# Optimization experiments

Measured on AMD Instinct MI355X. Metric: run time of the kernel, lower is better.

The kernel has to match this reference:

```python
import jax, jax.numpy as jnp
import numpy as np

H = 4
NEG_SLOPE = 0.2
N_P, N_A = 100000, 100000
E = 500000
L = 200000
F_IN, F_HID, F_OUT = 128, 128, 64


def setup_inputs() -> dict:
    key = jax.random.key(0)
    ks = jax.random.split(key, 32)
    s = 0.1  # weight init scale
    inp = {
        'x_paper': jax.random.normal(ks[0], (N_P, F_IN), jnp.float32),
        'x_author': jax.random.normal(ks[1], (N_A, F_IN), jnp.float32),
        'ei_pa': jax.random.randint(ks[2], (2, E), 0, N_P, jnp.int32),
        'ei_ap': jax.random.randint(ks[3], (2, E), 0, N_A, jnp.int32),
        'edge_label_index': jax.random.randint(ks[4], (2, L), 0, N_P, jnp.int32),
        # layer 1 params
        'p1W': s * jax.random.normal(ks[5], (F_IN, F_HID), jnp.float32),
        'p1b': jnp.zeros((F_HID,), jnp.float32),
        'a1W': s * jax.random.normal(ks[6], (F_IN, F_HID), jnp.float32),
        'a1b': jnp.zeros((F_HID,), jnp.float32),
        's1pa': s * jax.random.normal(ks[7], (H, F_HID // H), jnp.float32),
        'd1pa': s * jax.random.normal(ks[8], (H, F_HID // H), jnp.float32),
        's1ap': s * jax.random.normal(ks[9], (H, F_HID // H), jnp.float32),
        'd1ap': s * jax.random.normal(ks[10], (H, F_HID // H), jnp.float32),
        'k1W': s * jax.random.normal(ks[11], (F_HID, F_HID), jnp.float32),
        'k1b': jnp.zeros((F_HID,), jnp.float32),
        'q1': s * jax.random.normal(ks[12], (F_HID,), jnp.float32),
        # layer 2 params
        'p2W': s * jax.random.normal(ks[13], (F_HID, F_OUT), jnp.float32),
        'p2b': jnp.zeros((F_OUT,), jnp.float32),
        'a2W': s * jax.random.normal(ks[14], (F_HID, F_OUT), jnp.float32),
        'a2b': jnp.zeros((F_OUT,), jnp.float32),
        's2pa': s * jax.random.normal(ks[15], (H, F_OUT // H), jnp.float32),
        'd2pa': s * jax.random.normal(ks[16], (H, F_OUT // H), jnp.float32),
        's2ap': s * jax.random.normal(ks[17], (H, F_OUT // H), jnp.float32),
        'd2ap': s * jax.random.normal(ks[18], (H, F_OUT // H), jnp.float32),
        'k2W': s * jax.random.normal(ks[19], (F_OUT, F_OUT), jnp.float32),
        'k2b': jnp.zeros((F_OUT,), jnp.float32),
        'q2': s * jax.random.normal(ks[20], (F_OUT,), jnp.float32),
    }
    return inp


def _edge_attn(h_src, h_dst, src, dst, a_src, a_dst, num_dst):
    # h_*: [N, H, D]; a_*: [H, D]. Per-edge node-level GAT-style attention.
    alpha = (jnp.einsum('nhd,hd->nh', h_src, a_src)[src]
             + jnp.einsum('nhd,hd->nh', h_dst, a_dst)[dst])  # [E, H]
    alpha = jnp.where(alpha >= 0, alpha, NEG_SLOPE * alpha)  # leaky_relu
    amax = jax.ops.segment_max(alpha, dst, num_segments=num_dst)
    amax = jnp.where(jnp.isfinite(amax), amax, 0.0)
    ex = jnp.exp(alpha - amax[dst])
    denom = jax.ops.segment_sum(ex, dst, num_segments=num_dst)
    w = ex / (denom[dst] + 1e-16)
    out = jax.ops.segment_sum(h_src[src] * w[:, :, None], dst, num_segments=num_dst)
    return jax.nn.relu(out).reshape(num_dst, -1)  # [N_dst, H*D]


def _group(xs, q, kW, kb):
    # Semantic-level attention over metapaths (PyG HANConv `group`).
    out = jnp.stack(xs)  # [M, N, F]
    score = (q * jnp.tanh(out @ kW + kb).mean(axis=1)).sum(-1)  # [M]
    attn = jax.nn.softmax(score)
    return (attn[:, None, None] * out).sum(0)


def _han_layer(x_p, x_a, ei_pa, ei_ap, pW, pb, aW, ab, s_pa, d_pa, s_ap, d_ap, kW, kb, q):
    D = pW.shape[1] // H
    h_p = (x_p @ pW + pb).reshape(-1, H, D)
    h_a = (x_a @ aW + ab).reshape(-1, H, D)
    out_a = _edge_attn(h_p, h_a, ei_pa[0], ei_pa[1], s_pa, d_pa, h_a.shape[0])
    out_p = _edge_attn(h_a, h_p, ei_ap[0], ei_ap[1], s_ap, d_ap, h_p.shape[0])
    z_p = _group([out_p], q, kW, kb)
    z_a = _group([out_a], q, kW, kb)
    return z_p, z_a


def reference(x_paper, x_author, ei_pa, ei_ap, edge_label_index,
              p1W, p1b, a1W, a1b, s1pa, d1pa, s1ap, d1ap, k1W, k1b, q1,
              p2W, p2b, a2W, a2b, s2pa, d2pa, s2ap, d2ap, k2W, k2b, q2):
    z_p, z_a = _han_layer(x_paper, x_author, ei_pa, ei_ap,
                          p1W, p1b, a1W, a1b, s1pa, d1pa, s1ap, d1ap, k1W, k1b, q1)
    z_p, z_a = _han_layer(z_p, z_a, ei_pa, ei_ap,
                          p2W, p2b, a2W, a2b, s2pa, d2pa, s2ap, d2ap, k2W, k2b, q2)
    src = z_p[edge_label_index[0]]
    dst = z_a[edge_label_index[1]]
    return (src * dst).sum(axis=-1)  # [L]
```

## Files before the change

### kernel.cpp

```cpp
#include <hip/hip_runtime.h>


#define HEADS 4

typedef _Float16 f16x8 __attribute__((ext_vector_type(8)));
typedef _Float16 f16x4 __attribute__((ext_vector_type(4)));
typedef float    f32x4 __attribute__((ext_vector_type(4)));

__device__ __forceinline__ float leaky02(float a) {
    return a >= 0.f ? a : 0.2f * a;
}

__device__ __forceinline__ void prep_one(const float* W, _Float16* Wf, int M, int o) {
    const int NT = M / 16;
    const int v = o & 7, lane = (o >> 3) & 63, jt = o >> 9;
    const int t = jt / NT, j = jt % NT;
    const int k = t * 32 + (lane >> 4) * 8 + v;
    const int n = j * 16 + (lane & 15);
    Wf[o] = (_Float16)W[k * M + n];
}

__global__ __launch_bounds__(256) void prep_w4(
    const float* __restrict__ W1, _Float16* __restrict__ Wf1,
    const float* __restrict__ W2, _Float16* __restrict__ Wf2,
    const float* __restrict__ W3, _Float16* __restrict__ Wf3,
    const float* __restrict__ W4, _Float16* __restrict__ Wf4) {
    int o = blockIdx.x * 256 + threadIdx.x;
    if (o < 16384)       prep_one(W1, Wf1, 128, o);
    else if (o < 32768)  prep_one(W2, Wf2, 128, o - 16384);
    else if (o < 40960)  prep_one(W3, Wf3, 64, o - 32768);
    else if (o < 49152)  prep_one(W4, Wf4, 64, o - 40960);
}

template<int M, bool AHALF>
__global__ __launch_bounds__(256) void gemm_mfma_dual(
    const void* __restrict__ XA, const _Float16* __restrict__ WfA,
    const float* __restrict__ bA, _Float16* __restrict__ outA,
    const void* __restrict__ XB, const _Float16* __restrict__ WfB,
    const float* __restrict__ bB, _Float16* __restrict__ outB,
    int N, int nbHalf) {
    constexpr int NT = M / 16;
    __shared__ _Float16 stage[4][16][M + 4];

    const bool second = blockIdx.x >= nbHalf;
    const void* __restrict__ X        = second ? XB : XA;
    const _Float16* __restrict__ Wf   = second ? WfB : WfA;
    const float* __restrict__ b       = second ? bB : bA;
    _Float16* __restrict__ out        = second ? outB : outA;
    const int brow = second ? blockIdx.x - nbHalf : blockIdx.x;

    const int wave = threadIdx.x >> 6;
    const int lane = threadIdx.x & 63;
    const int row0 = (brow * 4 + wave) * 16;
    const int m    = lane & 15;
    const int quad = lane >> 4;

    f32x4 acc[NT];
    #pragma unroll
    for (int j = 0; j < NT; ++j) acc[j] = (f32x4){0.f, 0.f, 0.f, 0.f};

    int arow = row0 + m;
    if (arow >= N) arow = N - 1;

    #pragma unroll
    for (int t = 0; t < 4; ++t) {
        const int k0 = t * 32 + quad * 8;
        f16x8 a;
        if (AHALF) {
            a = *(const f16x8*)((const _Float16*)X + (size_t)arow * 128 + k0);
        } else {
            const float* xp = (const float*)X + (size_t)arow * 128 + k0;
            float4 v0 = *(const float4*)xp;
            float4 v1 = *(const float4*)(xp + 4);
            a = (f16x8){(_Float16)v0.x, (_Float16)v0.y, (_Float16)v0.z, (_Float16)v0.w,
                        (_Float16)v1.x, (_Float16)v1.y, (_Float16)v1.z, (_Float16)v1.w};
        }
        #pragma unroll
        for (int j = 0; j < NT; ++j) {
            f16x8 bf = *(const f16x8*)(Wf + ((size_t)(t * NT + j) * 64 + lane) * 8);
            acc[j] = __builtin_amdgcn_mfma_f32_16x16x32_f16(a, bf, acc[j], 0, 0, 0);
        }
    }

    #pragma unroll
    for (int j = 0; j < NT; ++j) {
        const float bias = b[j * 16 + m];
        #pragma unroll
        for (int r = 0; r < 4; ++r)
            stage[wave][quad * 4 + r][j * 16 + m] = (_Float16)(acc[j][r] + bias);
    }
    __syncthreads();

    constexpr int LPR = M / 4;
    constexpr int RPI = 64 / LPR;
    const int lr = lane % LPR;
    const int rq = lane / LPR;
    #pragma unroll
    for (int i = 0; i < 16 / RPI; ++i) {
        const int rr = i * RPI + rq;
        const int grow = row0 + rr;
        if (grow < N) {
            f16x4 v = *(const f16x4*)(&stage[wave][rr][lr * 4]);
            *(f16x4*)(out + (size_t)grow * M + lr * 4) = v;
        }
    }
}

template<int F, int D>
__global__ __launch_bounds__(256) void node_alpha_dual(
    const _Float16* __restrict__ hP, const float* __restrict__ sP,
    const float* __restrict__ dP, float* __restrict__ asP, float* __restrict__ adP,
    const _Float16* __restrict__ hA, const float* __restrict__ sA,
    const float* __restrict__ dA, float* __restrict__ asA, float* __restrict__ adA,
    int N) {
    constexpr int LPN = F / 4;
    constexpr int LPH = D / 4;
    const int gid    = blockIdx.x * blockDim.x + threadIdx.x;
    const int node_g = gid / LPN;
    const int lane   = gid % LPN;
    if (node_g >= 2 * N) return;
    const bool aut = node_g >= N;
    const int node = aut ? node_g - N : node_g;
    const _Float16* hbuf = aut ? hA : hP;
    const float* sv_p = aut ? sA : sP;
    const float* dv_p = aut ? dA : dP;
    float* as_p = aut ? asA : asP;
    float* ad_p = aut ? adA : adP;

    const int f0 = lane * 4;
    f16x4 h4 = *(const f16x4*)(hbuf + (size_t)node * F + f0);
    float4 sv = *(const float4*)(sv_p + f0);
    float4 dv = *(const float4*)(dv_p + f0);
    const float h0 = (float)h4[0], h1 = (float)h4[1], h2 = (float)h4[2], h3 = (float)h4[3];
    float ps = h0 * sv.x + h1 * sv.y + h2 * sv.z + h3 * sv.w;
    float pd = h0 * dv.x + h1 * dv.y + h2 * dv.z + h3 * dv.w;
    #pragma unroll
    for (int off = LPH >> 1; off > 0; off >>= 1) {
        ps += __shfl_xor(ps, off);
        pd += __shfl_xor(pd, off);
    }
    if ((lane % LPH) == 0) {
        int h = lane / LPH;
        as_p[(size_t)node * HEADS + h] = ps;
        ad_p[(size_t)node * HEADS + h] = pd;
    }
}

__global__ __launch_bounds__(256) void hist_dual(
    const int* __restrict__ dst_pa, const int* __restrict__ dst_ap,
    int* __restrict__ counts, int N, int E) {
    const int eg = blockIdx.x * 256 + threadIdx.x;
    if (eg >= 2 * E) return;
    const int idx = (eg < E) ? dst_pa[eg] : (N + dst_ap[eg - E]);
    atomicAdd(counts + idx, 1);
}

__global__ __launch_bounds__(256) void scan_blk(
    const int* __restrict__ in, int* __restrict__ out,
    int* __restrict__ bsum, int N) {
    __shared__ int sh[256];
    const int base = blockIdx.x * 1024 + threadIdx.x * 4;
    int v[4]; int s = 0;
    #pragma unroll
    for (int j = 0; j < 4; ++j) { v[j] = (base + j < N) ? in[base + j] : 0; s += v[j]; }
    sh[threadIdx.x] = s;
    __syncthreads();
    for (int off = 1; off < 256; off <<= 1) {
        int t = (threadIdx.x >= off) ? sh[threadIdx.x - off] : 0;
        __syncthreads();
        sh[threadIdx.x] += t;
        __syncthreads();
    }
    int run = sh[threadIdx.x] - s;
    #pragma unroll
    for (int j = 0; j < 4; ++j) {
        if (base + j < N) out[base + j] = run;
        run += v[j];
    }
    if (threadIdx.x == 255) bsum[blockIdx.x] = sh[255];
}

__global__ __launch_bounds__(256) void scan_sums(int* __restrict__ bsum, int nb) {
    __shared__ int sh[256];
    int v = (threadIdx.x < nb) ? bsum[threadIdx.x] : 0;
    sh[threadIdx.x] = v;
    __syncthreads();
    for (int off = 1; off < 256; off <<= 1) {
        int t = (threadIdx.x >= off) ? sh[threadIdx.x - off] : 0;
        __syncthreads();
        sh[threadIdx.x] += t;
        __syncthreads();
    }
    if (threadIdx.x < nb) bsum[threadIdx.x] = sh[threadIdx.x] - v;
}

__global__ __launch_bounds__(256) void scan_add(
    int* __restrict__ out, const int* __restrict__ bsum, int N) {
    const int base = blockIdx.x * 1024 + threadIdx.x * 4;
    const int add = bsum[blockIdx.x];
    #pragma unroll
    for (int j = 0; j < 4; ++j)
        if (base + j < N) out[base + j] += add;
}

__global__ __launch_bounds__(256) void scatter_dual(
    const int* __restrict__ src_pa, const int* __restrict__ dst_pa,
    const int* __restrict__ src_ap, const int* __restrict__ dst_ap,
    const int* __restrict__ offsets, int* __restrict__ cursor,
    int* __restrict__ perm, int N, int E) {
    const int eg = blockIdx.x * 256 + threadIdx.x;
    if (eg >= 2 * E) return;
    int idx, val;
    if (eg < E) { idx = dst_pa[eg];         val = src_pa[eg]; }
    else        { idx = N + dst_ap[eg - E]; val = src_ap[eg - E]; }
    const int pos = offsets[idx] + atomicAdd(cursor + idx, 1);
    perm[pos] = val;
}

template<int F, int D>
__global__ __launch_bounds__(256) void csr_attn_agg_dual(
    const int* __restrict__ perm, const int* __restrict__ offsets,
    const int* __restrict__ counts,
    const float* __restrict__ asrcP, const float* __restrict__ adstP,
    const _Float16* __restrict__ hP, _Float16* __restrict__ outA,
    const float* __restrict__ asrcA, const float* __restrict__ adstA,
    const _Float16* __restrict__ hA, _Float16* __restrict__ outP,
    int N) {
    constexpr int LPN = F / 4;
    const int gid    = blockIdx.x * 256 + threadIdx.x;
    const int node_g = gid / LPN;
    const int lane   = gid % LPN;
    if (node_g >= 2 * N) return;
    const bool second = node_g >= N;
    const int node = second ? node_g - N : node_g;
    const float* __restrict__ asrc    = second ? asrcA : asrcP;
    const float* __restrict__ adst    = second ? adstA : adstP;
    const _Float16* __restrict__ hsrc = second ? hA : hP;
    _Float16* __restrict__ out        = second ? outP : outA;

    const int start = offsets[node_g];
    const int cnt   = counts[node_g];
    const int f0 = lane * 4;
    const int h  = f0 / D;
    const float ad = adst[(size_t)node * HEADS + h];

    float den = 0.f;
    float4 acc = make_float4(0.f, 0.f, 0.f, 0.f);
    for (int i = 0; i < cnt; ++i) {
        int s = perm[start + i];
        float a = leaky02(asrc[(size_t)s * HEADS + h] + ad);
        float ex = __expf(a);
        den += ex;
        f16x4 hv = *(const f16x4*)(hsrc + (size_t)s * F + f0);
        acc.x += ex * (float)hv[0]; acc.y += ex * (float)hv[1];
        acc.z += ex * (float)hv[2]; acc.w += ex * (float)hv[3];
    }
    const float inv = 1.f / (den + 1e-16f);
    f16x4 o;
    o[0] = (_Float16)fmaxf(acc.x * inv, 0.f);
    o[1] = (_Float16)fmaxf(acc.y * inv, 0.f);
    o[2] = (_Float16)fmaxf(acc.z * inv, 0.f);
    o[3] = (_Float16)fmaxf(acc.w * inv, 0.f);
    *(f16x4*)(out + (size_t)node * F + f0) = o;
}

__global__ __launch_bounds__(256) void edge_dot(
    const int* __restrict__ eli, const _Float16* __restrict__ zp,
    const _Float16* __restrict__ za, float* __restrict__ out, int L) {
    constexpr int LPE = 16;
    const int gid  = blockIdx.x * blockDim.x + threadIdx.x;
    const int e    = gid / LPE;
    const int lane = gid % LPE;
    if (e >= L) return;
    const int p = eli[e], a = eli[(size_t)L + e];
    f16x4 pv = *(const f16x4*)(zp + (size_t)p * 64 + lane * 4);
    f16x4 av = *(const f16x4*)(za + (size_t)a * 64 + lane * 4);
    float s = (float)pv[0] * (float)av[0] + (float)pv[1] * (float)av[1]
            + (float)pv[2] * (float)av[2] + (float)pv[3] * (float)av[3];
    #pragma unroll
    for (int off = 8; off > 0; off >>= 1) s += __shfl_xor(s, off);
    if (lane == 0) out[e] = s;
}

static inline int cdiv(long long a, long long b) { return (int)((a + b - 1) / b); }

extern "C" void kernel_launch(void* const* d_in, const int* in_sizes, int n_in,
                              void* d_out, int out_size, void* d_ws, size_t ws_size,
                              hipStream_t stream) {
    const float* x_p  = (const float*)d_in[0];
    const float* x_a  = (const float*)d_in[1];
    const int* ei_pa  = (const int*)d_in[2];
    const int* ei_ap  = (const int*)d_in[3];
    const int* eli    = (const int*)d_in[4];
    const float* p1W = (const float*)d_in[5];
    const float* p1b = (const float*)d_in[6];
    const float* a1W = (const float*)d_in[7];
    const float* a1b = (const float*)d_in[8];
    const float* s1pa = (const float*)d_in[9];
    const float* d1pa = (const float*)d_in[10];
    const float* s1ap = (const float*)d_in[11];
    const float* d1ap = (const float*)d_in[12];
    const float* p2W = (const float*)d_in[16];
    const float* p2b = (const float*)d_in[17];
    const float* a2W = (const float*)d_in[18];
    const float* a2b = (const float*)d_in[19];
    const float* s2pa = (const float*)d_in[20];
    const float* d2pa = (const float*)d_in[21];
    const float* s2ap = (const float*)d_in[22];
    const float* d2ap = (const float*)d_in[23];

    const int NP = in_sizes[0] / 128;
    const int E  = in_sizes[2] / 2;
    const int L  = in_sizes[4] / 2;
    const int N  = NP;

    char* ws = (char*)d_ws;
    size_t off = 0;
    auto alloc = [&](size_t bytes) -> char* {
        char* p = ws + off;
        off += (bytes + 255) & ~(size_t)255;
        return p;
    };
    _Float16* h_p1   = (_Float16*)alloc((size_t)N * 128 * 2);
    _Float16* h_a1   = (_Float16*)alloc((size_t)N * 128 * 2);
    _Float16* out_p1 = (_Float16*)alloc((size_t)N * 128 * 2);
    _Float16* out_a1 = (_Float16*)alloc((size_t)N * 128 * 2);
    _Float16* h_p2   = (_Float16*)alloc((size_t)N * 64 * 2);
    _Float16* h_a2   = (_Float16*)alloc((size_t)N * 64 * 2);
    _Float16* out_p2 = (_Float16*)alloc((size_t)N * 64 * 2);
    _Float16* out_a2 = (_Float16*)alloc((size_t)N * 64 * 2);
    float* asrc_pa = (float*)alloc((size_t)N * HEADS * 4);
    float* adst_pa = (float*)alloc((size_t)N * HEADS * 4);
    float* asrc_ap = (float*)alloc((size_t)N * HEADS * 4);
    float* adst_ap = (float*)alloc((size_t)N * HEADS * 4);
    _Float16* Wf1p = (_Float16*)alloc(16384 * 2);
    _Float16* Wf1a = (_Float16*)alloc(16384 * 2);
    _Float16* Wf2p = (_Float16*)alloc(8192 * 2);
    _Float16* Wf2a = (_Float16*)alloc(8192 * 2);
    int* cnt2    = (int*)alloc((size_t)2 * N * 4);
    int* cursor2 = (int*)alloc((size_t)2 * N * 4);
    int* off2    = (int*)alloc((size_t)2 * N * 4);
    int* perm2   = (int*)alloc((size_t)2 * E * 4);
    int* bsum    = (int*)alloc(256 * 4);

    const int* src_pa = ei_pa;
    const int* dst_pa = ei_pa + E;
    const int* src_ap = ei_ap;
    const int* dst_ap = ei_ap + E;

    const int N2 = 2 * N;
    const int nbScan = cdiv(N2, 1024);

    prep_w4<<<cdiv(49152, 256), 256, 0, stream>>>(p1W, Wf1p, a1W, Wf1a, p2W, Wf2p, a2W, Wf2a);
    hipMemsetAsync(cnt2, 0, (size_t)4 * N * 4, stream);
    hist_dual<<<cdiv((long long)2 * E, 256), 256, 0, stream>>>(dst_pa, dst_ap, cnt2, N, E);
    scan_blk<<<nbScan, 256, 0, stream>>>(cnt2, off2, bsum, N2);
    scan_sums<<<1, 256, 0, stream>>>(bsum, nbScan);
    scan_add<<<nbScan, 256, 0, stream>>>(off2, bsum, N2);
    scatter_dual<<<cdiv((long long)2 * E, 256), 256, 0, stream>>>(
        src_pa, dst_pa, src_ap, dst_ap, off2, cursor2, perm2, N, E);

    const int nbHalf = cdiv(N, 64);

    gemm_mfma_dual<128, false><<<2 * nbHalf, 256, 0, stream>>>(
        x_p, Wf1p, p1b, h_p1, x_a, Wf1a, a1b, h_a1, N, nbHalf);
    node_alpha_dual<128, 32><<<cdiv((long long)N2 * 32, 256), 256, 0, stream>>>(
        h_p1, s1pa, d1ap, asrc_pa, adst_ap,
        h_a1, s1ap, d1pa, asrc_ap, adst_pa, N);
    csr_attn_agg_dual<128, 32><<<cdiv((long long)N2 * 32, 256), 256, 0, stream>>>(
        perm2, off2, cnt2,
        asrc_pa, adst_pa, h_p1, out_a1,
        asrc_ap, adst_ap, h_a1, out_p1, N);

    gemm_mfma_dual<64, true><<<2 * nbHalf, 256, 0, stream>>>(
        out_p1, Wf2p, p2b, h_p2, out_a1, Wf2a, a2b, h_a2, N, nbHalf);
    node_alpha_dual<64, 16><<<cdiv((long long)N2 * 16, 256), 256, 0, stream>>>(
        h_p2, s2pa, d2ap, asrc_pa, adst_ap,
        h_a2, s2ap, d2pa, asrc_ap, adst_pa, N);
    csr_attn_agg_dual<64, 16><<<cdiv((long long)N2 * 16, 256), 256, 0, stream>>>(
        perm2, off2, cnt2,
        asrc_pa, adst_pa, h_p2, out_a2,
        asrc_ap, adst_ap, h_a2, out_p2, N);

    edge_dot<<<cdiv((long long)L * 16, 256), 256, 0, stream>>>(
        eli, out_p2, out_a2, (float*)d_out, L);
}
```

Before: 476.2 us.

## Fuse node attention logits into GEMM, degree-sort aggregation, unroll edge loop

The per-node attention logit computation moves into the GEMM epilogue, reading the staged fp16 tile from shared memory, and the separate node_alpha kernels are removed. That saves a launch and a full re-read of h per layer. A degree counting sort (histogram, scan, scatter) builds a node order so aggregation threads in the same wave handle nodes of similar in-degree, which reduces divergence. The aggregation edge loop is unrolled by four to put more gathers in flight. In exchange the change adds three small kernels. The GEMM epilogue drops the __syncthreads, which relies on each wave reading only its own stage slice. The bhist buffer is assumed contiguous after cursor2 so the memset clears it.

```diff
diff --git a/kernel.cpp b/kernel.cpp
--- a/kernel.cpp
+++ b/kernel.cpp
@@ -36,17 +36,26 @@
 __global__ __launch_bounds__(256) void gemm_mfma_dual(
     const void* __restrict__ XA, const _Float16* __restrict__ WfA,
     const float* __restrict__ bA, _Float16* __restrict__ outA,
+    const float* __restrict__ svA, const float* __restrict__ dvA,
+    float* __restrict__ asA, float* __restrict__ adA,
     const void* __restrict__ XB, const _Float16* __restrict__ WfB,
     const float* __restrict__ bB, _Float16* __restrict__ outB,
+    const float* __restrict__ svB, const float* __restrict__ dvB,
+    float* __restrict__ asB, float* __restrict__ adB,
     int N, int nbHalf) {
     constexpr int NT = M / 16;
+    constexpr int D  = M / HEADS;
     __shared__ _Float16 stage[4][16][M + 4];
 
     const bool second = blockIdx.x >= nbHalf;
-    const void* __restrict__ X        = second ? XB : XA;
-    const _Float16* __restrict__ Wf   = second ? WfB : WfA;
-    const float* __restrict__ b       = second ? bB : bA;
-    _Float16* __restrict__ out        = second ? outB : outA;
+    const void* __restrict__ X      = second ? XB : XA;
+    const _Float16* __restrict__ Wf = second ? WfB : WfA;
+    const float* __restrict__ b     = second ? bB : bA;
+    _Float16* __restrict__ out      = second ? outB : outA;
+    const float* __restrict__ sv    = second ? svB : svA;
+    const float* __restrict__ dv    = second ? dvB : dvA;
+    float* __restrict__ asb         = second ? asB : asA;
+    float* __restrict__ adb         = second ? adB : adA;
     const int brow = second ? blockIdx.x - nbHalf : blockIdx.x;
 
     const int wave = threadIdx.x >> 6;
@@ -89,7 +98,27 @@
         for (int r = 0; r < 4; ++r)
             stage[wave][quad * 4 + r][j * 16 + m] = (_Float16)(acc[j][r] + bias);
     }
-    __syncthreads();
+
+    {
+        const int r  = lane >> 2;
+        const int hh = lane & 3;
+        float ps = 0.f, pd = 0.f;
+        #pragma unroll
+        for (int j = 0; j < D / 4; ++j) {
+            f16x4 v4 = *(const f16x4*)(&stage[wave][r][hh * D + 4 * j]);
+            float4 s4 = *(const float4*)(sv + hh * D + 4 * j);
+            float4 d4 = *(const float4*)(dv + hh * D + 4 * j);
+            const float v0 = (float)v4[0], v1 = (float)v4[1],
+                        v2 = (float)v4[2], v3 = (float)v4[3];
+            ps += v0 * s4.x + v1 * s4.y + v2 * s4.z + v3 * s4.w;
+            pd += v0 * d4.x + v1 * d4.y + v2 * d4.z + v3 * d4.w;
+        }
+        const int grow = row0 + r;
+        if (grow < N) {
+            asb[(size_t)grow * HEADS + hh] = ps;
+            adb[(size_t)grow * HEADS + hh] = pd;
+        }
+    }
 
     constexpr int LPR = M / 4;
     constexpr int RPI = 64 / LPR;
@@ -103,46 +132,6 @@
             f16x4 v = *(const f16x4*)(&stage[wave][rr][lr * 4]);
             *(f16x4*)(out + (size_t)grow * M + lr * 4) = v;
         }
-    }
-}
-
-template<int F, int D>
-__global__ __launch_bounds__(256) void node_alpha_dual(
-    const _Float16* __restrict__ hP, const float* __restrict__ sP,
-    const float* __restrict__ dP, float* __restrict__ asP, float* __restrict__ adP,
-    const _Float16* __restrict__ hA, const float* __restrict__ sA,
-    const float* __restrict__ dA, float* __restrict__ asA, float* __restrict__ adA,
-    int N) {
-    constexpr int LPN = F / 4;
-    constexpr int LPH = D / 4;
-    const int gid    = blockIdx.x * blockDim.x + threadIdx.x;
-    const int node_g = gid / LPN;
-    const int lane   = gid % LPN;
-    if (node_g >= 2 * N) return;
-    const bool aut = node_g >= N;
-    const int node = aut ? node_g - N : node_g;
-    const _Float16* hbuf = aut ? hA : hP;
-    const float* sv_p = aut ? sA : sP;
-    const float* dv_p = aut ? dA : dP;
-    float* as_p = aut ? asA : asP;
-    float* ad_p = aut ? adA : adP;
-
-    const int f0 = lane * 4;
-    f16x4 h4 = *(const f16x4*)(hbuf + (size_t)node * F + f0);
-    float4 sv = *(const float4*)(sv_p + f0);
-    float4 dv = *(const float4*)(dv_p + f0);
-    const float h0 = (float)h4[0], h1 = (float)h4[1], h2 = (float)h4[2], h3 = (float)h4[3];
-    float ps = h0 * sv.x + h1 * sv.y + h2 * sv.z + h3 * sv.w;
-    float pd = h0 * dv.x + h1 * dv.y + h2 * dv.z + h3 * dv.w;
-    #pragma unroll
-    for (int off = LPH >> 1; off > 0; off >>= 1) {
-        ps += __shfl_xor(ps, off);
-        pd += __shfl_xor(pd, off);
-    }
-    if ((lane % LPH) == 0) {
-        int h = lane / LPH;
-        as_p[(size_t)node * HEADS + h] = ps;
-        ad_p[(size_t)node * HEADS + h] = pd;
     }
 }
 
@@ -217,8 +206,42 @@
     perm[pos] = val;
 }
 
+__global__ __launch_bounds__(256) void deg_hist(
+    const int* __restrict__ cnt, int* __restrict__ bhist, int n) {
+    __shared__ int lh[64];
+    if (threadIdx.x < 64) lh[threadIdx.x] = 0;
+    __syncthreads();
+    for (int i = blockIdx.x * 256 + threadIdx.x; i < n; i += gridDim.x * 256) {
+        int c = cnt[i]; if (c > 63) c = 63;
+        atomicAdd(&lh[c], 1);
+    }
+    __syncthreads();
+    if (threadIdx.x < 64) atomicAdd(&bhist[threadIdx.x], lh[threadIdx.x]);
+}
+
+__global__ __launch_bounds__(256) void deg_scatter(
+    const int* __restrict__ cnt, int* __restrict__ bcur,
+    int* __restrict__ order, int n) {
+    __shared__ int lh[64];
+    __shared__ int lbase[64];
+    if (threadIdx.x < 64) lh[threadIdx.x] = 0;
+    __syncthreads();
+    const int i = blockIdx.x * 256 + threadIdx.x;
+    int c = 0, lpos = 0;
+    if (i < n) {
+        c = cnt[i]; if (c > 63) c = 63;
+        lpos = atomicAdd(&lh[c], 1);
+    }
+    __syncthreads();
+    if (threadIdx.x < 64 && lh[threadIdx.x] > 0)
+        lbase[threadIdx.x] = atomicAdd(&bcur[threadIdx.x], lh[threadIdx.x]);
+    __syncthreads();
+    if (i < n) order[lbase[c] + lpos] = i;
+}
+
 template<int F, int D>
 __global__ __launch_bounds__(256) void csr_attn_agg_dual(
+    const int* __restrict__ order,
     const int* __restrict__ perm, const int* __restrict__ offsets,
     const int* __restrict__ counts,
     const float* __restrict__ asrcP, const float* __restrict__ adstP,
@@ -227,10 +250,11 @@
     const _Float16* __restrict__ hA, _Float16* __restrict__ outP,
     int N) {
     constexpr int LPN = F / 4;
-    const int gid    = blockIdx.x * 256 + threadIdx.x;
-    const int node_g = gid / LPN;
-    const int lane   = gid % LPN;
-    if (node_g >= 2 * N) return;
+    const int gid  = blockIdx.x * 256 + threadIdx.x;
+    const int slot = gid / LPN;
+    const int lane = gid % LPN;
+    if (slot >= 2 * N) return;
+    const int node_g = order[slot];
     const bool second = node_g >= N;
     const int node = second ? node_g - N : node_g;
     const float* __restrict__ asrc    = second ? asrcA : asrcP;
@@ -246,10 +270,34 @@
 
     float den = 0.f;
     float4 acc = make_float4(0.f, 0.f, 0.f, 0.f);
-    for (int i = 0; i < cnt; ++i) {
-        int s = perm[start + i];
-        float a = leaky02(asrc[(size_t)s * HEADS + h] + ad);
-        float ex = __expf(a);
+    int i = 0;
+    for (; i + 4 <= cnt; i += 4) {
+        const int s0 = perm[start + i + 0];
+        const int s1 = perm[start + i + 1];
+        const int s2 = perm[start + i + 2];
+        const int s3 = perm[start + i + 3];
+        const float a0 = asrc[(size_t)s0 * HEADS + h];
+        const float a1 = asrc[(size_t)s1 * HEADS + h];
+        const float a2 = asrc[(size_t)s2 * HEADS + h];
+        const float a3 = asrc[(size_t)s3 * HEADS + h];
+        f16x4 h0 = *(const f16x4*)(hsrc + (size_t)s0 * F + f0);
+        f16x4 h1 = *(const f16x4*)(hsrc + (size_t)s1 * F + f0);
+        f16x4 h2 = *(const f16x4*)(hsrc + (size_t)s2 * F + f0);
+        f16x4 h3 = *(const f16x4*)(hsrc + (size_t)s3 * F + f0);
+        const float e0 = __expf(leaky02(a0 + ad));
+        const float e1 = __expf(leaky02(a1 + ad));
+        const float e2 = __expf(leaky02(a2 + ad));
+        const float e3 = __expf(leaky02(a3 + ad));
+        den += (e0 + e1) + (e2 + e3);
+        acc.x += e0 * (float)h0[0] + e1 * (float)h1[0] + e2 * (float)h2[0] + e3 * (float)h3[0];
+        acc.y += e0 * (float)h0[1] + e1 * (float)h1[1] + e2 * (float)h2[1] + e3 * (float)h3[1];
+        acc.z += e0 * (float)h0[2] + e1 * (float)h1[2] + e2 * (float)h2[2] + e3 * (float)h3[2];
+        acc.w += e0 * (float)h0[3] + e1 * (float)h1[3] + e2 * (float)h2[3] + e3 * (float)h3[3];
+    }
+    for (; i < cnt; ++i) {
+        const int s = perm[start + i];
+        const float a = leaky02(asrc[(size_t)s * HEADS + h] + ad);
+        const float ex = __expf(a);
         den += ex;
         f16x4 hv = *(const f16x4*)(hsrc + (size_t)s * F + f0);
         acc.x += ex * (float)hv[0]; acc.y += ex * (float)hv[1];
@@ -339,8 +387,10 @@
     _Float16* Wf2a = (_Float16*)alloc(8192 * 2);
     int* cnt2    = (int*)alloc((size_t)2 * N * 4);
     int* cursor2 = (int*)alloc((size_t)2 * N * 4);
+    int* bhist   = (int*)alloc(256);
     int* off2    = (int*)alloc((size_t)2 * N * 4);
     int* perm2   = (int*)alloc((size_t)2 * E * 4);
+    int* order2  = (int*)alloc((size_t)2 * N * 4);
     int* bsum    = (int*)alloc(256 * 4);
 
     const int* src_pa = ei_pa;
@@ -352,33 +402,32 @@
     const int nbScan = cdiv(N2, 1024);
 
     prep_w4<<<cdiv(49152, 256), 256, 0, stream>>>(p1W, Wf1p, a1W, Wf1a, p2W, Wf2p, a2W, Wf2a);
-    hipMemsetAsync(cnt2, 0, (size_t)4 * N * 4, stream);
+    hipMemsetAsync(cnt2, 0, ((size_t)4 * N + 64) * 4, stream);
     hist_dual<<<cdiv((long long)2 * E, 256), 256, 0, stream>>>(dst_pa, dst_ap, cnt2, N, E);
     scan_blk<<<nbScan, 256, 0, stream>>>(cnt2, off2, bsum, N2);
     scan_sums<<<1, 256, 0, stream>>>(bsum, nbScan);
     scan_add<<<nbScan, 256, 0, stream>>>(off2, bsum, N2);
     scatter_dual<<<cdiv((long long)2 * E, 256), 256, 0, stream>>>(
         src_pa, dst_pa, src_ap, dst_ap, off2, cursor2, perm2, N, E);
+    deg_hist<<<256, 256, 0, stream>>>(cnt2, bhist, N2);
+    scan_sums<<<1, 256, 0, stream>>>(bhist, 64);
+    deg_scatter<<<cdiv(N2, 256), 256, 0, stream>>>(cnt2, bhist, order2, N2);
 
     const int nbHalf = cdiv(N, 64);
 
     gemm_mfma_dual<128, false><<<2 * nbHalf, 256, 0, stream>>>(
-        x_p, Wf1p, p1b, h_p1, x_a, Wf1a, a1b, h_a1, N, nbHalf);
-    node_alpha_dual<128, 32><<<cdiv((long long)N2 * 32, 256), 256, 0, stream>>>(
-        h_p1, s1pa, d1ap, asrc_pa, adst_ap,
-        h_a1, s1ap, d1pa, asrc_ap, adst_pa, N);
+        x_p, Wf1p, p1b, h_p1, s1pa, d1ap, asrc_pa, adst_ap,
+        x_a, Wf1a, a1b, h_a1, s1ap, d1pa, asrc_ap, adst_pa, N, nbHalf);
     csr_attn_agg_dual<128, 32><<<cdiv((long long)N2 * 32, 256), 256, 0, stream>>>(
-        perm2, off2, cnt2,
+        order2, perm2, off2, cnt2,
         asrc_pa, adst_pa, h_p1, out_a1,
         asrc_ap, adst_ap, h_a1, out_p1, N);
 
     gemm_mfma_dual<64, true><<<2 * nbHalf, 256, 0, stream>>>(
-        out_p1, Wf2p, p2b, h_p2, out_a1, Wf2a, a2b, h_a2, N, nbHalf);
-    node_alpha_dual<64, 16><<<cdiv((long long)N2 * 16, 256), 256, 0, stream>>>(
-        h_p2, s2pa, d2ap, asrc_pa, adst_ap,
-        h_a2, s2ap, d2pa, asrc_ap, adst_pa, N);
+        out_p1, Wf2p, p2b, h_p2, s2pa, d2ap, asrc_pa, adst_ap,
+        out_a1, Wf2a, a2b, h_a2, s2ap, d2pa, asrc_ap, adst_pa, N, nbHalf);
     csr_attn_agg_dual<64, 16><<<cdiv((long long)N2 * 16, 256), 256, 0, stream>>>(
-        perm2, off2, cnt2,
+        order2, perm2, off2, cnt2,
         asrc_pa, adst_pa, h_p2, out_a2,
         asrc_ap, adst_ap, h_a2, out_p2, N);
 
```

After: 465.2 us. 2.3% less time.
